# Kernel optimization log

Measured on AMD Instinct MI355X. Metric: run time of the kernel, lower is better.

## Reference

```python
import jax, jax.numpy as jnp
import numpy as np

N = 100_000       # nodes
E = 600_000       # edges
D_IN = 128
D_OUT = 128


def setup_inputs() -> dict:
    key = jax.random.key(0)
    k0, k1, k2, k3, k4, k5 = jax.random.split(key, 6)
    node_feature = jax.random.normal(k0, (N, D_IN), dtype=jnp.float32)
    edge_index = jax.random.randint(k1, (2, E), 0, N, dtype=jnp.int32)
    s = 1.0 / np.sqrt(D_IN)  # torch nn.Linear default init range
    W1 = jax.random.uniform(k2, (D_OUT, D_IN), jnp.float32, -s, s)
    b1 = jax.random.uniform(k3, (D_OUT,), jnp.float32, -s, s)
    W2 = jax.random.uniform(k4, (D_OUT, D_IN), jnp.float32, -s, s)
    b2 = jax.random.uniform(k5, (D_OUT,), jnp.float32, -s, s)
    return {"node_feature": node_feature, "edge_index": edge_index,
            "W1": W1, "b1": b1, "W2": W2, "b2": b2}


def reference(node_feature, edge_index, W1, b1, W2, b2):
    # h1 = lin1(x)
    h1 = node_feature @ W1.T + b1                       # [N, D_OUT]
    src, dst = edge_index[0], edge_index[1]
    # scatter(x[src], dst, reduce='mul', dim_size=N): segment product,
    # identity 1 for nodes with no incoming edges
    msgs = node_feature[src]                            # [E, D_IN]
    aggr = jax.ops.segment_prod(msgs, dst, num_segments=N)  # [N, D_IN]
    h2 = aggr @ W2.T + b2                               # [N, D_OUT]
    return h1 * h2
```

## Files before the change

### kernel.cpp

```cpp
#include <hip/hip_runtime.h>

#define NN 100000
#define NE 600000
#define D  128
#define CAP 64
#define NT (NN / 16)

typedef __attribute__((ext_vector_type(8))) short short8;
typedef __attribute__((ext_vector_type(4))) float floatx4;

__device__ __forceinline__ unsigned short f2bf(float f) {
    union { float f; unsigned int u; } a; a.f = f;
    unsigned int r = a.u + 0x7fff + ((a.u >> 16) & 1);
    return (unsigned short)(r >> 16);
}
__device__ __forceinline__ float bf2f(unsigned short h) {
    union { unsigned int u; float f; } a; a.u = ((unsigned int)h) << 16;
    return a.f;
}

__global__ __launch_bounds__(256) void prep_kernel(const float* __restrict__ W1,
                                                   const float* __restrict__ W2,
                                                   short8* __restrict__ wfrag,
                                                   int* __restrict__ counts) {
    int idx = blockIdx.x * 256 + threadIdx.x;
    for (int j = idx; j < NN; j += 4096) counts[j] = 0;

    int m2 = idx >> 11;
    int rem = idx & 2047;
    int c = rem >> 8;
    int q = (rem >> 6) & 3;
    int l = rem & 63;
    const float* W = m2 ? W2 : W1;
    int row = c * 16 + (l & 15);
    int kb = q * 32 + 8 * (l >> 4);
    const float* src = &W[row * D + kb];
    short8 h, lo;
#pragma unroll
    for (int j = 0; j < 8; ++j) {
        float v = src[j];
        unsigned short hh = f2bf(v);
        h[j]  = (short)hh;
        lo[j] = (short)f2bf(v - bf2f(hh));
    }
    wfrag[(((m2 * 2 + 0) * 8 + c) * 4 + q) * 64 + l] = h;
    wfrag[(((m2 * 2 + 1) * 8 + c) * 4 + q) * 64 + l] = lo;
}


__global__ void bucket_kernel(const int* __restrict__ src, const int* __restrict__ dst,
                              int* __restrict__ counts, int* __restrict__ bucket, int e) {
    int i = blockIdx.x * blockDim.x + threadIdx.x;
    if (i < e) {
        int d = dst[i];
        int pos = atomicAdd(&counts[d], 1);
        if (pos < CAP) bucket[(size_t)d * CAP + pos] = src[i];
    }
}

__global__ __launch_bounds__(512, 1)
void fused_kernel(const float* __restrict__ x,
                  const int* __restrict__ counts,
                  const int* __restrict__ bucket,
                  const short8* __restrict__ wfrag,
                  const float* __restrict__ b1,
                  const float* __restrict__ b2,
                  float* __restrict__ out) {
    __shared__ short8 sW[2 * 8 * 4 * 64];

    const int lane = threadIdx.x & 63;
    const int wv   = threadIdx.x >> 6;
    const int r16  = lane & 15;
    const int g    = lane >> 4;

    const int tile = blockIdx.x * 8 + wv;
    const bool live = (tile < NT);
    const int base = tile * 16;
    const size_t rowoff = live ? ((size_t)(base + r16) * D + g * 8) : 0;

    for (int i = threadIdx.x; i < 4096; i += 512) sW[i] = wfrag[i];

    floatx4 p[8];
#pragma unroll
    for (int k = 0; k < 8; ++k) p[k] = (floatx4)1.f;
    if (live) {
        const int node = base + r16;
        int cnt = counts[node]; if (cnt > CAP) cnt = CAP;
        const int* bp = &bucket[(size_t)node * CAP];
        for (int ib = 0; ib < cnt; ib += 8) {
            int4 ia = *(const int4*)&bp[ib];
            int4 ic = *(const int4*)&bp[ib + 4];
            int s8[8] = { ia.x, ia.y, ia.z, ia.w, ic.x, ic.y, ic.z, ic.w };
            int m = cnt - ib;
#pragma unroll
            for (int j = 0; j < 8; ++j) {
                if (j < m) {
                    const float* xr = &x[(size_t)s8[j] * D + g * 8];
#pragma unroll
                    for (int q = 0; q < 4; ++q) {
                        p[2 * q]     *= *(const floatx4*)&xr[q * 32];
                        p[2 * q + 1] *= *(const floatx4*)&xr[q * 32 + 4];
                    }
                }
            }
        }
    }
    short8 gh[4], gl[4];
#pragma unroll
    for (int q = 0; q < 4; ++q) {
        short8 h, l;
#pragma unroll
        for (int jj = 0; jj < 4; ++jj) {
            unsigned short hh = f2bf(p[2 * q][jj]);
            h[jj] = (short)hh;
            l[jj] = (short)f2bf(p[2 * q][jj] - bf2f(hh));
            unsigned short hh2 = f2bf(p[2 * q + 1][jj]);
            h[4 + jj] = (short)hh2;
            l[4 + jj] = (short)f2bf(p[2 * q + 1][jj] - bf2f(hh2));
        }
        gh[q] = h; gl[q] = l;
    }

    __syncthreads();

    floatx4 acc[8];
#pragma unroll
    for (int c = 0; c < 8; ++c) acc[c] = (floatx4)0.f;

    floatx4 h1[8];
    if (live) {
        const float* xr = &x[rowoff];
#pragma unroll
        for (int q = 0; q < 4; ++q) {
            floatx4 v0 = *(const floatx4*)&xr[q * 32];
            floatx4 v1 = *(const floatx4*)&xr[q * 32 + 4];
            short8 fh, fl;
#pragma unroll
            for (int jj = 0; jj < 4; ++jj) {
                unsigned short hh = f2bf(v0[jj]);
                fh[jj] = (short)hh;
                fl[jj] = (short)f2bf(v0[jj] - bf2f(hh));
                unsigned short hh2 = f2bf(v1[jj]);
                fh[4 + jj] = (short)hh2;
                fl[4 + jj] = (short)f2bf(v1[jj] - bf2f(hh2));
            }
#pragma unroll
            for (int c = 0; c < 8; ++c) {
                short8 bh = sW[((0 * 8 + c) * 4 + q) * 64 + lane];
                short8 bl = sW[((1 * 8 + c) * 4 + q) * 64 + lane];
                acc[c] = __builtin_amdgcn_mfma_f32_16x16x32_bf16(fh, bh, acc[c], 0, 0, 0);
                acc[c] = __builtin_amdgcn_mfma_f32_16x16x32_bf16(fl, bh, acc[c], 0, 0, 0);
                acc[c] = __builtin_amdgcn_mfma_f32_16x16x32_bf16(fh, bl, acc[c], 0, 0, 0);
            }
        }
#pragma unroll
        for (int c = 0; c < 8; ++c) {
            float bb = b1[c * 16 + r16];
            floatx4 t = acc[c];
            t[0] += bb; t[1] += bb; t[2] += bb; t[3] += bb;
            h1[c] = t;
            acc[c] = (floatx4)0.f;
        }
    }

    __syncthreads();
    for (int i = threadIdx.x; i < 4096; i += 512) sW[i] = wfrag[4096 + i];
    __syncthreads();

    if (live) {
#pragma unroll
        for (int q = 0; q < 4; ++q) {
#pragma unroll
            for (int c = 0; c < 8; ++c) {
                short8 bh = sW[((0 * 8 + c) * 4 + q) * 64 + lane];
                short8 bl = sW[((1 * 8 + c) * 4 + q) * 64 + lane];
                acc[c] = __builtin_amdgcn_mfma_f32_16x16x32_bf16(gh[q], bh, acc[c], 0, 0, 0);
                acc[c] = __builtin_amdgcn_mfma_f32_16x16x32_bf16(gl[q], bh, acc[c], 0, 0, 0);
                acc[c] = __builtin_amdgcn_mfma_f32_16x16x32_bf16(gh[q], bl, acc[c], 0, 0, 0);
            }
        }
#pragma unroll
        for (int c = 0; c < 8; ++c) {
            float bb = b2[c * 16 + r16];
#pragma unroll
            for (int r = 0; r < 4; ++r) {
                out[(size_t)(base + g * 4 + r) * D + c * 16 + r16] =
                    h1[c][r] * (acc[c][r] + bb);
            }
        }
    }
}


extern "C" void kernel_launch(void* const* d_in, const int* in_sizes, int n_in,
                              void* d_out, int out_size, void* d_ws, size_t ws_size,
                              hipStream_t stream) {
    const float* x  = (const float*)d_in[0];
    const int*   ei = (const int*)d_in[1];
    const float* W1 = (const float*)d_in[2];
    const float* b1 = (const float*)d_in[3];
    const float* W2 = (const float*)d_in[4];
    const float* b2 = (const float*)d_in[5];
    float* out = (float*)d_out;

    const int n = NN, e = NE;
    const int* src = ei;
    const int* dst = ei + e;

    char* ws = (char*)d_ws;
    short8* wfrag = (short8*)ws;                ws += 8192 * 16;
    int* counts = (int*)ws;                     ws += (size_t)n * sizeof(int);
    ws += 256 - ((uintptr_t)ws & 255);
    int* bucket = (int*)ws;

    prep_kernel<<<16, 256, 0, stream>>>(W1, W2, wfrag, counts);
    bucket_kernel<<<(e + 255) / 256, 256, 0, stream>>>(src, dst, counts, bucket, e);
    fused_kernel<<<(NT + 7) / 8, 512, 0, stream>>>(x, counts, bucket, wfrag, b1, b2, out);
}
```

Measured before the change: 125.8 us.

## Make fused kernel persistent with both weight sets resident in LDS

The fused kernel becomes a persistent grid of 256 blocks of 1024 threads. Each block loads both W1 and W2 bf16 fragments into LDS once (128 KB) and then loops over node tiles, which removes the per-block weight reload and the mid-kernel barriers. The bucket kernel now handles four edges per thread using int4 loads. In exchange, occupancy drops to one large block per CU, so fewer waves are available to hide gather latency, and load balance across tiles becomes static.

```diff
diff --git a/kernel.cpp b/kernel.cpp
--- a/kernel.cpp
+++ b/kernel.cpp
@@ -50,15 +50,25 @@
 
 __global__ void bucket_kernel(const int* __restrict__ src, const int* __restrict__ dst,
                               int* __restrict__ counts, int* __restrict__ bucket, int e) {
-    int i = blockIdx.x * blockDim.x + threadIdx.x;
-    if (i < e) {
-        int d = dst[i];
-        int pos = atomicAdd(&counts[d], 1);
-        if (pos < CAP) bucket[(size_t)d * CAP + pos] = src[i];
+    int i = (blockIdx.x * blockDim.x + threadIdx.x) * 4;
+    if (i + 4 <= e) {
+        int4 d4 = *(const int4*)&dst[i];
+        int4 s4 = *(const int4*)&src[i];
+        int pos;
+        pos = atomicAdd(&counts[d4.x], 1); if (pos < CAP) bucket[(size_t)d4.x * CAP + pos] = s4.x;
+        pos = atomicAdd(&counts[d4.y], 1); if (pos < CAP) bucket[(size_t)d4.y * CAP + pos] = s4.y;
+        pos = atomicAdd(&counts[d4.z], 1); if (pos < CAP) bucket[(size_t)d4.z * CAP + pos] = s4.z;
+        pos = atomicAdd(&counts[d4.w], 1); if (pos < CAP) bucket[(size_t)d4.w * CAP + pos] = s4.w;
+    } else {
+        for (; i < e; ++i) {
+            int d = dst[i];
+            int pos = atomicAdd(&counts[d], 1);
+            if (pos < CAP) bucket[(size_t)d * CAP + pos] = src[i];
+        }
     }
 }
 
-__global__ __launch_bounds__(512, 1)
+__global__ __launch_bounds__(1024, 1)
 void fused_kernel(const float* __restrict__ x,
                   const int* __restrict__ counts,
                   const int* __restrict__ bucket,
@@ -66,93 +76,93 @@
                   const float* __restrict__ b1,
                   const float* __restrict__ b2,
                   float* __restrict__ out) {
-    __shared__ short8 sW[2 * 8 * 4 * 64];
+    __shared__ short8 sW[8192];
+    for (int i = threadIdx.x; i < 8192; i += 1024) sW[i] = wfrag[i];
 
     const int lane = threadIdx.x & 63;
     const int wv   = threadIdx.x >> 6;
     const int r16  = lane & 15;
     const int g    = lane >> 4;
 
-    const int tile = blockIdx.x * 8 + wv;
-    const bool live = (tile < NT);
-    const int base = tile * 16;
-    const size_t rowoff = live ? ((size_t)(base + r16) * D + g * 8) : 0;
-
-    for (int i = threadIdx.x; i < 4096; i += 512) sW[i] = wfrag[i];
-
-    floatx4 p[8];
-#pragma unroll
-    for (int k = 0; k < 8; ++k) p[k] = (floatx4)1.f;
-    if (live) {
-        const int node = base + r16;
-        int cnt = counts[node]; if (cnt > CAP) cnt = CAP;
-        const int* bp = &bucket[(size_t)node * CAP];
-        for (int ib = 0; ib < cnt; ib += 8) {
-            int4 ia = *(const int4*)&bp[ib];
-            int4 ic = *(const int4*)&bp[ib + 4];
-            int s8[8] = { ia.x, ia.y, ia.z, ia.w, ic.x, ic.y, ic.z, ic.w };
-            int m = cnt - ib;
-#pragma unroll
-            for (int j = 0; j < 8; ++j) {
-                if (j < m) {
-                    const float* xr = &x[(size_t)s8[j] * D + g * 8];
-#pragma unroll
-                    for (int q = 0; q < 4; ++q) {
-                        p[2 * q]     *= *(const floatx4*)&xr[q * 32];
-                        p[2 * q + 1] *= *(const floatx4*)&xr[q * 32 + 4];
+    __syncthreads();
+
+    const int stride = gridDim.x * 16;
+    for (int tile = blockIdx.x * 16 + wv; tile < NT; tile += stride) {
+        const int base = tile * 16;
+        const size_t rowoff = (size_t)(base + r16) * D + g * 8;
+
+        floatx4 p[8];
+#pragma unroll
+        for (int k = 0; k < 8; ++k) p[k] = (floatx4)1.f;
+        {
+            const int node = base + r16;
+            int cnt = counts[node]; if (cnt > CAP) cnt = CAP;
+            const int* bp = &bucket[(size_t)node * CAP];
+            for (int ib = 0; ib < cnt; ib += 8) {
+                int4 ia = *(const int4*)&bp[ib];
+                int4 ic = *(const int4*)&bp[ib + 4];
+                int s8[8] = { ia.x, ia.y, ia.z, ia.w, ic.x, ic.y, ic.z, ic.w };
+                int m = cnt - ib;
+#pragma unroll
+                for (int j = 0; j < 8; ++j) {
+                    if (j < m) {
+                        const float* xr = &x[(size_t)s8[j] * D + g * 8];
+#pragma unroll
+                        for (int q = 0; q < 4; ++q) {
+                            p[2 * q]     *= *(const floatx4*)&xr[q * 32];
+                            p[2 * q + 1] *= *(const floatx4*)&xr[q * 32 + 4];
+                        }
                     }
                 }
             }
         }
-    }
-    short8 gh[4], gl[4];
-#pragma unroll
-    for (int q = 0; q < 4; ++q) {
-        short8 h, l;
-#pragma unroll
-        for (int jj = 0; jj < 4; ++jj) {
-            unsigned short hh = f2bf(p[2 * q][jj]);
-            h[jj] = (short)hh;
-            l[jj] = (short)f2bf(p[2 * q][jj] - bf2f(hh));
-            unsigned short hh2 = f2bf(p[2 * q + 1][jj]);
-            h[4 + jj] = (short)hh2;
-            l[4 + jj] = (short)f2bf(p[2 * q + 1][jj] - bf2f(hh2));
-        }
-        gh[q] = h; gl[q] = l;
-    }
-
-    __syncthreads();
-
-    floatx4 acc[8];
-#pragma unroll
-    for (int c = 0; c < 8; ++c) acc[c] = (floatx4)0.f;
-
-    floatx4 h1[8];
-    if (live) {
-        const float* xr = &x[rowoff];
+        short8 gh[4], gl[4];
 #pragma unroll
         for (int q = 0; q < 4; ++q) {
-            floatx4 v0 = *(const floatx4*)&xr[q * 32];
-            floatx4 v1 = *(const floatx4*)&xr[q * 32 + 4];
-            short8 fh, fl;
+            short8 h, l;
 #pragma unroll
             for (int jj = 0; jj < 4; ++jj) {
-                unsigned short hh = f2bf(v0[jj]);
-                fh[jj] = (short)hh;
-                fl[jj] = (short)f2bf(v0[jj] - bf2f(hh));
-                unsigned short hh2 = f2bf(v1[jj]);
-                fh[4 + jj] = (short)hh2;
-                fl[4 + jj] = (short)f2bf(v1[jj] - bf2f(hh2));
-            }
-#pragma unroll
-            for (int c = 0; c < 8; ++c) {
-                short8 bh = sW[((0 * 8 + c) * 4 + q) * 64 + lane];
-                short8 bl = sW[((1 * 8 + c) * 4 + q) * 64 + lane];
-                acc[c] = __builtin_amdgcn_mfma_f32_16x16x32_bf16(fh, bh, acc[c], 0, 0, 0);
-                acc[c] = __builtin_amdgcn_mfma_f32_16x16x32_bf16(fl, bh, acc[c], 0, 0, 0);
-                acc[c] = __builtin_amdgcn_mfma_f32_16x16x32_bf16(fh, bl, acc[c], 0, 0, 0);
-            }
-        }
+                unsigned short hh = f2bf(p[2 * q][jj]);
+                h[jj] = (short)hh;
+                l[jj] = (short)f2bf(p[2 * q][jj] - bf2f(hh));
+                unsigned short hh2 = f2bf(p[2 * q + 1][jj]);
+                h[4 + jj] = (short)hh2;
+                l[4 + jj] = (short)f2bf(p[2 * q + 1][jj] - bf2f(hh2));
+            }
+            gh[q] = h; gl[q] = l;
+        }
+
+        floatx4 acc[8];
+#pragma unroll
+        for (int c = 0; c < 8; ++c) acc[c] = (floatx4)0.f;
+
+        {
+            const float* xr = &x[rowoff];
+#pragma unroll
+            for (int q = 0; q < 4; ++q) {
+                floatx4 v0 = *(const floatx4*)&xr[q * 32];
+                floatx4 v1 = *(const floatx4*)&xr[q * 32 + 4];
+                short8 fh, fl;
+#pragma unroll
+                for (int jj = 0; jj < 4; ++jj) {
+                    unsigned short hh = f2bf(v0[jj]);
+                    fh[jj] = (short)hh;
+                    fl[jj] = (short)f2bf(v0[jj] - bf2f(hh));
+                    unsigned short hh2 = f2bf(v1[jj]);
+                    fh[4 + jj] = (short)hh2;
+                    fl[4 + jj] = (short)f2bf(v1[jj] - bf2f(hh2));
+                }
+#pragma unroll
+                for (int c = 0; c < 8; ++c) {
+                    short8 bh = sW[((0 * 8 + c) * 4 + q) * 64 + lane];
+                    short8 bl = sW[((1 * 8 + c) * 4 + q) * 64 + lane];
+                    acc[c] = __builtin_amdgcn_mfma_f32_16x16x32_bf16(fh, bh, acc[c], 0, 0, 0);
+                    acc[c] = __builtin_amdgcn_mfma_f32_16x16x32_bf16(fl, bh, acc[c], 0, 0, 0);
+                    acc[c] = __builtin_amdgcn_mfma_f32_16x16x32_bf16(fh, bl, acc[c], 0, 0, 0);
+                }
+            }
+        }
+        floatx4 h1[8];
 #pragma unroll
         for (int c = 0; c < 8; ++c) {
             float bb = b1[c * 16 + r16];
@@ -161,19 +171,13 @@
             h1[c] = t;
             acc[c] = (floatx4)0.f;
         }
-    }
-
-    __syncthreads();
-    for (int i = threadIdx.x; i < 4096; i += 512) sW[i] = wfrag[4096 + i];
-    __syncthreads();
-
-    if (live) {
+
 #pragma unroll
         for (int q = 0; q < 4; ++q) {
 #pragma unroll
             for (int c = 0; c < 8; ++c) {
-                short8 bh = sW[((0 * 8 + c) * 4 + q) * 64 + lane];
-                short8 bl = sW[((1 * 8 + c) * 4 + q) * 64 + lane];
+                short8 bh = sW[4096 + ((0 * 8 + c) * 4 + q) * 64 + lane];
+                short8 bl = sW[4096 + ((1 * 8 + c) * 4 + q) * 64 + lane];
                 acc[c] = __builtin_amdgcn_mfma_f32_16x16x32_bf16(gh[q], bh, acc[c], 0, 0, 0);
                 acc[c] = __builtin_amdgcn_mfma_f32_16x16x32_bf16(gl[q], bh, acc[c], 0, 0, 0);
                 acc[c] = __builtin_amdgcn_mfma_f32_16x16x32_bf16(gh[q], bl, acc[c], 0, 0, 0);
@@ -214,6 +218,6 @@
     int* bucket = (int*)ws;
 
     prep_kernel<<<16, 256, 0, stream>>>(W1, W2, wfrag, counts);
-    bucket_kernel<<<(e + 255) / 256, 256, 0, stream>>>(src, dst, counts, bucket, e);
-    fused_kernel<<<(NT + 7) / 8, 512, 0, stream>>>(x, counts, bucket, wfrag, b1, b2, out);
-}
+    bucket_kernel<<<(e / 4 + 255) / 256, 256, 0, stream>>>(src, dst, counts, bucket, e);
+    fused_kernel<<<256, 1024, 0, stream>>>(x, counts, bucket, wfrag, b1, b2, out);
+}
```

Measured after the change: 476.5 us. 3.79x slower.
